# Kernel optimization log

Measured on AMD Instinct MI355X. Metric: run time of the kernel, lower is better.

## Reference

```python
import jax, jax.numpy as jnp
import numpy as np

LAYER_NUM = 4
INPUT_DIM = 1024
BATCH = 16384


def setup_inputs() -> dict:
    key = jax.random.key(0)
    k1, k2, k3 = jax.random.split(key, 3)
    x = jax.random.normal(k1, (BATCH, INPUT_DIM), dtype=jnp.float32)
    cross_weights = jax.random.normal(k2, (LAYER_NUM, INPUT_DIM), dtype=jnp.float32)
    cross_bias = jax.random.normal(k3, (LAYER_NUM, INPUT_DIM), dtype=jnp.float32)
    return {"x": x, "cross_weights": cross_weights, "cross_bias": cross_bias}


def reference(x, cross_weights, cross_bias):
    # Faithful DCN cross network:
    #   x_{i+1} = x0 @ x_i^T @ w_i + b_i + x_i
    # The [B,d,d] outer product bmm collapses to a per-row scalar dot:
    #   x_{i+1} = x0 * (x_i . w_i) + b_i + x_i
    x0 = x
    xi = x
    for i in range(LAYER_NUM):
        s = xi @ cross_weights[i]            # [B]  (x_i^T w_i)
        xi = x0 * s[:, None] + cross_bias[i] + xi  # [B, d]
    return xi
```

## Files before the change

kernel.cpp:

```cpp
#include <hip/hip_runtime.h>


#define D 1024
#define NV4 (D / 4)
#define RPW 4
#define LPR 16
#define CPL (NV4 / LPR)

typedef float nfloat4 __attribute__((ext_vector_type(4)));

__global__ __launch_bounds__(256, 4) void cross_v3_kernel(
    const float* __restrict__ x,
    const float* __restrict__ w,
    const float* __restrict__ b,
    float* __restrict__ out,
    int batch)
{
    __shared__ float4 ldsB[4][NV4];

    const int tid  = (int)threadIdx.x;
    const int wvid = tid >> 6;
    const int lane = tid & 63;
    const int wid  = (int)blockIdx.x * 4 + wvid;
    const int row0 = wid * RPW;
    if (row0 >= batch) return;

    const int r = lane >> 4;
    const int t = lane & 15;
    int rr = row0 + r;
    if (rr >= batch) rr = batch - 1;
    const int row = rr;

    const float4* xr = (const float4*)x + (size_t)row * NV4;
    float4 xv[CPL];
#pragma unroll
    for (int c = 0; c < CPL; ++c) xv[c] = xr[c * LPR + t];

    const float4* w4 = (const float4*)w;
    const float4* b4 = (const float4*)b;

    float g1 = 0.f, g2 = 0.f, g3 = 0.f;
#pragma unroll
    for (int c = 0; c < 4; ++c) {
        const int idx = c * 64 + lane;
        float4 bb0 = b4[idx], bb1 = b4[256 + idx];
        float4 bb2 = b4[512 + idx], bb3 = b4[768 + idx];
        float4 wv1 = w4[256 + idx], wv2 = w4[512 + idx], wv3 = w4[768 + idx];

        float4 B2, B3, Bs;
        B2.x = bb0.x + bb1.x; B2.y = bb0.y + bb1.y;
        B2.z = bb0.z + bb1.z; B2.w = bb0.w + bb1.w;
        B3.x = B2.x + bb2.x;  B3.y = B2.y + bb2.y;
        B3.z = B2.z + bb2.z;  B3.w = B2.w + bb2.w;
        Bs.x = B3.x + bb3.x;  Bs.y = B3.y + bb3.y;
        Bs.z = B3.z + bb3.z;  Bs.w = B3.w + bb3.w;
        ldsB[wvid][idx] = Bs;

        g1 = fmaf(bb0.x, wv1.x, g1); g1 = fmaf(bb0.y, wv1.y, g1);
        g1 = fmaf(bb0.z, wv1.z, g1); g1 = fmaf(bb0.w, wv1.w, g1);
        g2 = fmaf(B2.x,  wv2.x, g2); g2 = fmaf(B2.y,  wv2.y, g2);
        g2 = fmaf(B2.z,  wv2.z, g2); g2 = fmaf(B2.w,  wv2.w, g2);
        g3 = fmaf(B3.x,  wv3.x, g3); g3 = fmaf(B3.y,  wv3.y, g3);
        g3 = fmaf(B3.z,  wv3.z, g3); g3 = fmaf(B3.w,  wv3.w, g3);
    }

#pragma unroll
    for (int off = 32; off > 0; off >>= 1) {
        g1 += __shfl_xor(g1, off, 64);
        g2 += __shfl_xor(g2, off, 64);
        g3 += __shfl_xor(g3, off, 64);
    }

    float d0 = 0.f, d1 = 0.f, d2 = 0.f, d3 = 0.f;
#pragma unroll
    for (int c = 0; c < CPL; ++c) {
        const int wi = c * LPR + t;
        float4 wv0 = w4[wi];
        float4 wv1 = w4[256 + wi];
        float4 wv2 = w4[512 + wi];
        float4 wv3 = w4[768 + wi];
        float4 xc = xv[c];
        d0 = fmaf(xc.x, wv0.x, d0); d1 = fmaf(xc.x, wv1.x, d1);
        d2 = fmaf(xc.x, wv2.x, d2); d3 = fmaf(xc.x, wv3.x, d3);
        d0 = fmaf(xc.y, wv0.y, d0); d1 = fmaf(xc.y, wv1.y, d1);
        d2 = fmaf(xc.y, wv2.y, d2); d3 = fmaf(xc.y, wv3.y, d3);
        d0 = fmaf(xc.z, wv0.z, d0); d1 = fmaf(xc.z, wv1.z, d1);
        d2 = fmaf(xc.z, wv2.z, d2); d3 = fmaf(xc.z, wv3.z, d3);
        d0 = fmaf(xc.w, wv0.w, d0); d1 = fmaf(xc.w, wv1.w, d1);
        d2 = fmaf(xc.w, wv2.w, d2); d3 = fmaf(xc.w, wv3.w, d3);
    }

#pragma unroll
    for (int off = 8; off > 0; off >>= 1) {
        d0 += __shfl_xor(d0, off, 64);
        d1 += __shfl_xor(d1, off, 64);
        d2 += __shfl_xor(d2, off, 64);
        d3 += __shfl_xor(d3, off, 64);
    }

    const float c1 = 1.f + d0;
    const float c2 = c1 + fmaf(c1, d1, g1);
    const float c3 = c2 + fmaf(c2, d2, g2);
    const float c4 = c3 + fmaf(c3, d3, g3);

    nfloat4* orow = (nfloat4*)out + (size_t)row * NV4;
#pragma unroll
    for (int c = 0; c < CPL; ++c) {
        const int wi = c * LPR + t;
        float4 Bs = ldsB[wvid][wi];
        nfloat4 o;
        o.x = fmaf(c4, xv[c].x, Bs.x);
        o.y = fmaf(c4, xv[c].y, Bs.y);
        o.z = fmaf(c4, xv[c].z, Bs.z);
        o.w = fmaf(c4, xv[c].w, Bs.w);
        __builtin_nontemporal_store(o, &orow[wi]);
    }
}

extern "C" void kernel_launch(void* const* d_in, const int* in_sizes, int n_in,
                              void* d_out, int out_size, void* d_ws, size_t ws_size,
                              hipStream_t stream) {
    const float* x = (const float*)d_in[0];
    const float* w = (const float*)d_in[1];
    const float* b = (const float*)d_in[2];
    float* out = (float*)d_out;

    const int batch = in_sizes[0] / D;
    const int rows_per_block = RPW * (256 / 64);
    const int grid = (batch + rows_per_block - 1) / rows_per_block;
    cross_v3_kernel<<<grid, 256, 0, stream>>>(x, w, b, out, batch);
}
```

Before: 139.1 us.

## Precompute bias sums and bias-weight dots in a separate prep kernel

Moves the per-wave redundant computation of cumulative bias sums and bias-weight dot products into a one-block prep kernel that writes them to workspace. The main kernel reads those constants from global memory instead of recomputing them per wave and staging them in LDS. Rows per wave drop from 4 to 2 with 32 lanes per row, which doubles the grid. This adds a second launch and a serial dependency between the two kernels, and the Bs reads now come from global/L2 rather than LDS.

```diff
diff --git a/kernel.cpp b/kernel.cpp
--- a/kernel.cpp
+++ b/kernel.cpp
@@ -3,30 +3,74 @@
 
 #define D 1024
 #define NV4 (D / 4)
-#define RPW 4
-#define LPR 16
+#define RPW 2
+#define LPR 32
 #define CPL (NV4 / LPR)
 
 typedef float nfloat4 __attribute__((ext_vector_type(4)));
 
-__global__ __launch_bounds__(256, 4) void cross_v3_kernel(
+__global__ void cross_prep_kernel(const float* __restrict__ w,
+                                  const float* __restrict__ b,
+                                  float* __restrict__ ws)
+{
+    __shared__ float red[3][4];
+    const int t    = (int)threadIdx.x;
+    const int lane = t & 63;
+    const int wv   = t >> 6;
+
+    const float4* w4 = (const float4*)w;
+    const float4* b4 = (const float4*)b;
+
+    float4 bb0 = b4[t], bb1 = b4[256 + t], bb2 = b4[512 + t], bb3 = b4[768 + t];
+    float4 wv1 = w4[256 + t], wv2 = w4[512 + t], wv3 = w4[768 + t];
+
+    float4 B2, B3, Bs;
+    B2.x = bb0.x + bb1.x; B2.y = bb0.y + bb1.y;
+    B2.z = bb0.z + bb1.z; B2.w = bb0.w + bb1.w;
+    B3.x = B2.x + bb2.x;  B3.y = B2.y + bb2.y;
+    B3.z = B2.z + bb2.z;  B3.w = B2.w + bb2.w;
+    Bs.x = B3.x + bb3.x;  Bs.y = B3.y + bb3.y;
+    Bs.z = B3.z + bb3.z;  Bs.w = B3.w + bb3.w;
+    ((float4*)ws)[t] = Bs;
+
+    float g1 = 0.f, g2 = 0.f, g3 = 0.f;
+    g1 = fmaf(bb0.x, wv1.x, g1); g1 = fmaf(bb0.y, wv1.y, g1);
+    g1 = fmaf(bb0.z, wv1.z, g1); g1 = fmaf(bb0.w, wv1.w, g1);
+    g2 = fmaf(B2.x,  wv2.x, g2); g2 = fmaf(B2.y,  wv2.y, g2);
+    g2 = fmaf(B2.z,  wv2.z, g2); g2 = fmaf(B2.w,  wv2.w, g2);
+    g3 = fmaf(B3.x,  wv3.x, g3); g3 = fmaf(B3.y,  wv3.y, g3);
+    g3 = fmaf(B3.z,  wv3.z, g3); g3 = fmaf(B3.w,  wv3.w, g3);
+
+#pragma unroll
+    for (int off = 32; off > 0; off >>= 1) {
+        g1 += __shfl_xor(g1, off, 64);
+        g2 += __shfl_xor(g2, off, 64);
+        g3 += __shfl_xor(g3, off, 64);
+    }
+    if (lane == 0) { red[0][wv] = g1; red[1][wv] = g2; red[2][wv] = g3; }
+    __syncthreads();
+    if (t == 0) {
+        ws[1024] = red[0][0] + red[0][1] + red[0][2] + red[0][3];
+        ws[1025] = red[1][0] + red[1][1] + red[1][2] + red[1][3];
+        ws[1026] = red[2][0] + red[2][1] + red[2][2] + red[2][3];
+    }
+}
+
+__global__ __launch_bounds__(256, 4) void cross_v4_kernel(
     const float* __restrict__ x,
     const float* __restrict__ w,
-    const float* __restrict__ b,
+    const float* __restrict__ ws,
     float* __restrict__ out,
     int batch)
 {
-    __shared__ float4 ldsB[4][NV4];
-
     const int tid  = (int)threadIdx.x;
-    const int wvid = tid >> 6;
     const int lane = tid & 63;
-    const int wid  = (int)blockIdx.x * 4 + wvid;
+    const int wid  = (int)blockIdx.x * 4 + (tid >> 6);
     const int row0 = wid * RPW;
     if (row0 >= batch) return;
 
-    const int r = lane >> 4;
-    const int t = lane & 15;
+    const int r = lane >> 5;
+    const int t = lane & 31;
     int rr = row0 + r;
     if (rr >= batch) rr = batch - 1;
     const int row = rr;
@@ -36,41 +80,9 @@
 #pragma unroll
     for (int c = 0; c < CPL; ++c) xv[c] = xr[c * LPR + t];
 
+    const float g1 = ws[1024], g2 = ws[1025], g3 = ws[1026];
+
     const float4* w4 = (const float4*)w;
-    const float4* b4 = (const float4*)b;
-
-    float g1 = 0.f, g2 = 0.f, g3 = 0.f;
-#pragma unroll
-    for (int c = 0; c < 4; ++c) {
-        const int idx = c * 64 + lane;
-        float4 bb0 = b4[idx], bb1 = b4[256 + idx];
-        float4 bb2 = b4[512 + idx], bb3 = b4[768 + idx];
-        float4 wv1 = w4[256 + idx], wv2 = w4[512 + idx], wv3 = w4[768 + idx];
-
-        float4 B2, B3, Bs;
-        B2.x = bb0.x + bb1.x; B2.y = bb0.y + bb1.y;
-        B2.z = bb0.z + bb1.z; B2.w = bb0.w + bb1.w;
-        B3.x = B2.x + bb2.x;  B3.y = B2.y + bb2.y;
-        B3.z = B2.z + bb2.z;  B3.w = B2.w + bb2.w;
-        Bs.x = B3.x + bb3.x;  Bs.y = B3.y + bb3.y;
-        Bs.z = B3.z + bb3.z;  Bs.w = B3.w + bb3.w;
-        ldsB[wvid][idx] = Bs;
-
-        g1 = fmaf(bb0.x, wv1.x, g1); g1 = fmaf(bb0.y, wv1.y, g1);
-        g1 = fmaf(bb0.z, wv1.z, g1); g1 = fmaf(bb0.w, wv1.w, g1);
-        g2 = fmaf(B2.x,  wv2.x, g2); g2 = fmaf(B2.y,  wv2.y, g2);
-        g2 = fmaf(B2.z,  wv2.z, g2); g2 = fmaf(B2.w,  wv2.w, g2);
-        g3 = fmaf(B3.x,  wv3.x, g3); g3 = fmaf(B3.y,  wv3.y, g3);
-        g3 = fmaf(B3.z,  wv3.z, g3); g3 = fmaf(B3.w,  wv3.w, g3);
-    }
-
-#pragma unroll
-    for (int off = 32; off > 0; off >>= 1) {
-        g1 += __shfl_xor(g1, off, 64);
-        g2 += __shfl_xor(g2, off, 64);
-        g3 += __shfl_xor(g3, off, 64);
-    }
-
     float d0 = 0.f, d1 = 0.f, d2 = 0.f, d3 = 0.f;
 #pragma unroll
     for (int c = 0; c < CPL; ++c) {
@@ -91,7 +103,7 @@
     }
 
 #pragma unroll
-    for (int off = 8; off > 0; off >>= 1) {
+    for (int off = 16; off > 0; off >>= 1) {
         d0 += __shfl_xor(d0, off, 64);
         d1 += __shfl_xor(d1, off, 64);
         d2 += __shfl_xor(d2, off, 64);
@@ -103,11 +115,12 @@
     const float c3 = c2 + fmaf(c2, d2, g2);
     const float c4 = c3 + fmaf(c3, d3, g3);
 
+    const float4* Bs4 = (const float4*)ws;
     nfloat4* orow = (nfloat4*)out + (size_t)row * NV4;
 #pragma unroll
     for (int c = 0; c < CPL; ++c) {
         const int wi = c * LPR + t;
-        float4 Bs = ldsB[wvid][wi];
+        float4 Bs = Bs4[wi];
         nfloat4 o;
         o.x = fmaf(c4, xv[c].x, Bs.x);
         o.y = fmaf(c4, xv[c].y, Bs.y);
@@ -124,9 +137,12 @@
     const float* w = (const float*)d_in[1];
     const float* b = (const float*)d_in[2];
     float* out = (float*)d_out;
+    float* ws  = (float*)d_ws;
 
     const int batch = in_sizes[0] / D;
     const int rows_per_block = RPW * (256 / 64);
     const int grid = (batch + rows_per_block - 1) / rows_per_block;
-    cross_v3_kernel<<<grid, 256, 0, stream>>>(x, w, b, out, batch);
+
+    cross_prep_kernel<<<1, 256, 0, stream>>>(w, b, ws);
+    cross_v4_kernel<<<grid, 256, 0, stream>>>(x, w, ws, out, batch);
 }
```

Measured after the change: 119.1 us. -14.3%, faster.
